# Optimization experiments

Measured on AMD Instinct MI355X. Metric: run time of the kernel, lower is better.

## Reference

```python
import jax, jax.numpy as jnp
import numpy as np

N, F, O, E = 2048, 128, 128, 16


def setup_inputs() -> dict:
    key = jax.random.key(0)
    ks = jax.random.split(key, 6)
    x = jax.random.normal(ks[0], (N, F), dtype=jnp.float32)
    # two supports (normalized adjacency-like dense matrices)
    support = jax.random.uniform(ks[1], (2, N, N), dtype=jnp.float32)
    edge_feature = jax.random.normal(ks[2], (N, N, E), dtype=jnp.float32)
    # glorot-ish scale for edge weight and dense weights
    weight_edge = jax.random.normal(ks[3], (N, N, E), dtype=jnp.float32) * 0.05
    bias_edge = jnp.zeros((N, N), dtype=jnp.float32)
    glorot = float(np.sqrt(6.0 / (F + O)))
    w0 = jax.random.uniform(ks[4], (F, O), dtype=jnp.float32, minval=-glorot, maxval=glorot)
    w1 = jax.random.uniform(ks[5], (F, O), dtype=jnp.float32, minval=-glorot, maxval=glorot)
    b = jnp.zeros((O,), dtype=jnp.float32)
    return {"x": x, "support": support, "edge_feature": edge_feature,
            "weight_edge": weight_edge, "bias_edge": bias_edge,
            "w0": w0, "w1": w1, "b": b}


def reference(x, support, edge_feature, weight_edge, bias_edge, w0, w1, b):
    # support branch 0: plain GCN propagation  (SpMM expressed dense)
    pre0 = x @ w0                      # [N, O]
    s0 = support[0] @ pre0             # [N, O]
    # support branch 1: edge-feature gated propagation
    pre1 = x @ w1                      # [N, O]
    # per-pair dot of edge features with per-pair weights -> [N, N] gate
    edge = jax.nn.sigmoid(jnp.einsum('nme,nme->nm', edge_feature, weight_edge) + bias_edge)
    s1 = (edge * support[1]) @ pre1    # gated adjacency matmul, [N, O]
    out = s0 + s1 + b                  # add_n + bias
    return jax.nn.relu(out)
```

## Files before the change

kernel.cpp:

```cpp
#include <hip/hip_runtime.h>
#include <math.h>

#define N 2048
#define F 128
#define O 128
#define E 16

#define BK 32
#define GBN 16
#define GKC 8
#define GMK (N / GKC)
#define GSTEPS (GMK / BK)

typedef __attribute__((ext_vector_type(8))) short          shortx8;
typedef __attribute__((ext_vector_type(8))) unsigned short u16x8;
typedef __attribute__((ext_vector_type(4))) float          floatx4;

static __device__ __forceinline__ unsigned short f2bf(float f) {
    unsigned int u = __float_as_uint(f);
    unsigned int r = (u + 0x7FFFu + ((u >> 16) & 1u)) >> 16;
    return (unsigned short)r;
}

__global__ __launch_bounds__(128)
void pre_gemm(const float* __restrict__ x,
              const float* __restrict__ w0,
              const float* __restrict__ w1,
              unsigned short* __restrict__ pre_bf) {
    const int n = blockIdx.x;
    const int b = blockIdx.y;
    const int o = threadIdx.x;
    const float* __restrict__ w = b ? w1 : w0;
    __shared__ float xs[F];
    xs[o] = x[(size_t)n * F + o];
    __syncthreads();
    float acc = 0.f;
#pragma unroll 8
    for (int k = 0; k < F; ++k)
        acc += xs[k] * w[(size_t)k * O + o];
    pre_bf[(size_t)b * N * O + (size_t)n * O + o] = f2bf(acc);
}

__global__ __launch_bounds__(256)
void transpose_pre(const unsigned short* __restrict__ pre_bf,
                   unsigned short* __restrict__ preT) {
    __shared__ unsigned short tile[64][65];
    const int n0 = blockIdx.x * 64, o0 = blockIdx.y * 64;
    const size_t base = (size_t)blockIdx.z * N * O;
    const int t = threadIdx.x;
    const int r = t >> 2, q = t & 3;
    const unsigned short* src = pre_bf + base + (size_t)(n0 + r) * O + o0 + q * 16;
    u16x8 v0 = *(const u16x8*)(src);
    u16x8 v1 = *(const u16x8*)(src + 8);
#pragma unroll
    for (int j = 0; j < 8; ++j) {
        tile[q * 16 + j][r]     = v0[j];
        tile[q * 16 + 8 + j][r] = v1[j];
    }
    __syncthreads();
    u16x8 w0v, w1v;
#pragma unroll
    for (int j = 0; j < 8; ++j) {
        w0v[j] = tile[r][q * 16 + j];
        w1v[j] = tile[r][q * 16 + 8 + j];
    }
    unsigned short* dst = preT + base + (size_t)(o0 + r) * N + n0 + q * 16;
    *(u16x8*)(dst)     = w0v;
    *(u16x8*)(dst + 8) = w1v;
}

__global__ __launch_bounds__(256)
void gate_kernel(const float* __restrict__ ef,
                 const float* __restrict__ we,
                 const float* __restrict__ be,
                 const float* __restrict__ sup1,
                 unsigned short* __restrict__ G) {
    const size_t tid  = (size_t)blockIdx.x * 256 + threadIdx.x;
    const size_t pair = tid >> 2;
    const int    sub  = (int)(threadIdx.x & 3);
    const float4 e4 = ((const float4*)ef)[pair * 4 + sub];
    const float4 w4 = ((const float4*)we)[pair * 4 + sub];
    float v = e4.x * w4.x + e4.y * w4.y + e4.z * w4.z + e4.w * w4.w;
    v += __shfl_xor(v, 1);
    v += __shfl_xor(v, 2);
    if (sub == 0) {
        const float t = v + be[pair];
        const float g = (1.f / (1.f + __expf(-t))) * sup1[pair];
        G[pair] = f2bf(g);
    }
}

__global__ __launch_bounds__(256)
void dual_gemm(const float* __restrict__ S0,
               const unsigned short* __restrict__ G,
               const unsigned short* __restrict__ preT,
               float* __restrict__ partial) {
    const int t    = threadIdx.x;
    const int lane = t & 63;
    const int w    = t >> 6;
    const int rb   = blockIdx.x & 127;
    const int kc   = blockIdx.x >> 7;
    const int n0   = rb * GBN;
    const int m_b  = kc * GMK;

    const int row  = lane & 15;
    const int kg   = lane >> 4;
    const int col0 = w * 32 + row;

    const float*          aS = S0   + (size_t)(n0 + row) * N + m_b + kg * 8;
    const unsigned short* aG = G    + (size_t)(n0 + row) * N + m_b + kg * 8;
    const unsigned short* b0 = preT + (size_t)col0 * N            + m_b + kg * 8;
    const unsigned short* b1 = b0   + (size_t)16 * N;
    const unsigned short* c0 = b0   + (size_t)O * N;
    const unsigned short* c1 = b1   + (size_t)O * N;

    floatx4 acc0 = {0.f, 0.f, 0.f, 0.f};
    floatx4 acc1 = {0.f, 0.f, 0.f, 0.f};

#pragma unroll 2
    for (int s = 0; s < GSTEPS; ++s) {
        const int mo = s * BK;
        const float4 f0 = *(const float4*)(aS + mo);
        const float4 f1 = *(const float4*)(aS + mo + 4);
        const shortx8 a_g = *(const shortx8*)(aG + mo);
        const shortx8 b00 = *(const shortx8*)(b0 + mo);
        const shortx8 b01 = *(const shortx8*)(b1 + mo);
        const shortx8 b10 = *(const shortx8*)(c0 + mo);
        const shortx8 b11 = *(const shortx8*)(c1 + mo);
        shortx8 a_s;
        a_s[0] = (short)f2bf(f0.x); a_s[1] = (short)f2bf(f0.y);
        a_s[2] = (short)f2bf(f0.z); a_s[3] = (short)f2bf(f0.w);
        a_s[4] = (short)f2bf(f1.x); a_s[5] = (short)f2bf(f1.y);
        a_s[6] = (short)f2bf(f1.z); a_s[7] = (short)f2bf(f1.w);
        acc0 = __builtin_amdgcn_mfma_f32_16x16x32_bf16(a_s, b00, acc0, 0, 0, 0);
        acc0 = __builtin_amdgcn_mfma_f32_16x16x32_bf16(a_g, b10, acc0, 0, 0, 0);
        acc1 = __builtin_amdgcn_mfma_f32_16x16x32_bf16(a_s, b01, acc1, 0, 0, 0);
        acc1 = __builtin_amdgcn_mfma_f32_16x16x32_bf16(a_g, b11, acc1, 0, 0, 0);
    }

    float* dst = partial + (size_t)kc * (N * O)
               + (size_t)(n0 + kg * 4) * O + w * 32 + row;
#pragma unroll
    for (int j = 0; j < 4; ++j) {
        dst[(size_t)j * O]      = acc0[j];
        dst[(size_t)j * O + 16] = acc1[j];
    }
}

__global__ __launch_bounds__(256)
void reduce_out(const float* __restrict__ partial,
                const float* __restrict__ bias,
                float* __restrict__ out) {
    const int i4 = blockIdx.x * 256 + threadIdx.x;
    const float4* p = (const float4*)partial;
    float4 r = p[i4];
#pragma unroll
    for (int j = 1; j < GKC; ++j) {
        const float4 a = p[i4 + (size_t)j * (N * O / 4)];
        r.x += a.x; r.y += a.y; r.z += a.z; r.w += a.w;
    }
    const float4 bb = ((const float4*)bias)[i4 & (O / 4 - 1)];
    float4 o;
    o.x = fmaxf(r.x + bb.x, 0.f);
    o.y = fmaxf(r.y + bb.y, 0.f);
    o.z = fmaxf(r.z + bb.z, 0.f);
    o.w = fmaxf(r.w + bb.w, 0.f);
    ((float4*)out)[i4] = o;
}

extern "C" void kernel_launch(void* const* d_in, const int* in_sizes, int n_in,
                              void* d_out, int out_size, void* d_ws, size_t ws_size,
                              hipStream_t stream) {
    const float* x   = (const float*)d_in[0];
    const float* sup = (const float*)d_in[1];
    const float* ef  = (const float*)d_in[2];
    const float* we  = (const float*)d_in[3];
    const float* be  = (const float*)d_in[4];
    const float* w0  = (const float*)d_in[5];
    const float* w1  = (const float*)d_in[6];
    const float* b   = (const float*)d_in[7];
    float* out = (float*)d_out;

    unsigned short* preT   = (unsigned short*)d_ws;
    unsigned short* G      = preT + 2 * (size_t)N * O;
    float*          partial = (float*)(G + (size_t)N * N);
    unsigned short* pre_bf = (unsigned short*)partial;

    pre_gemm<<<dim3(N, 2), 128, 0, stream>>>(x, w0, w1, pre_bf);
    transpose_pre<<<dim3(N / 64, O / 64, 2), 256, 0, stream>>>(pre_bf, preT);
    gate_kernel<<<(unsigned)((size_t)N * N * 4 / 256), 256, 0, stream>>>(
        ef, we, be, sup + (size_t)N * N, G);
    dual_gemm<<<GKC * 128, 256, 0, stream>>>(sup, G, preT, partial);
    reduce_out<<<N * O / 4 / 256, 256, 0, stream>>>(partial, b, out);
}
```

Before: 143.3 us.

## Fuse pre-GEMM with transpose via MFMA and do split-K reduction in-block

Replaces the scalar pre_gemm plus separate transpose kernel with one MFMA kernel that stages a bf16 transposed weight tile in LDS and writes the transposed pre-activation directly. The dual GEMM now splits K across the four waves of a block and reduces through shared memory, applying bias and ReLU in the same kernel. This removes the partial-sum buffer round trip and the reduce kernel, so two launches go away. Each block now covers only 32 output columns, so the S0 and G rows are re-read by four column-group blocks; a block index swizzle is added to improve cache locality for those re-reads.

```diff
diff --git a/kernel.cpp b/kernel.cpp
--- a/kernel.cpp
+++ b/kernel.cpp
@@ -6,14 +6,9 @@
 #define O 128
 #define E 16
 
-#define BK 32
-#define GBN 16
-#define GKC 8
-#define GMK (N / GKC)
-#define GSTEPS (GMK / BK)
-
 typedef __attribute__((ext_vector_type(8))) short          shortx8;
 typedef __attribute__((ext_vector_type(8))) unsigned short u16x8;
+typedef __attribute__((ext_vector_type(4))) unsigned short u16x4;
 typedef __attribute__((ext_vector_type(4))) float          floatx4;
 
 static __device__ __forceinline__ unsigned short f2bf(float f) {
@@ -22,51 +17,56 @@
     return (unsigned short)r;
 }
 
-__global__ __launch_bounds__(128)
-void pre_gemm(const float* __restrict__ x,
-              const float* __restrict__ w0,
-              const float* __restrict__ w1,
-              unsigned short* __restrict__ pre_bf) {
-    const int n = blockIdx.x;
-    const int b = blockIdx.y;
-    const int o = threadIdx.x;
-    const float* __restrict__ w = b ? w1 : w0;
-    __shared__ float xs[F];
-    xs[o] = x[(size_t)n * F + o];
-    __syncthreads();
-    float acc = 0.f;
-#pragma unroll 8
-    for (int k = 0; k < F; ++k)
-        acc += xs[k] * w[(size_t)k * O + o];
-    pre_bf[(size_t)b * N * O + (size_t)n * O + o] = f2bf(acc);
-}
+__global__ __launch_bounds__(256)
+void pre_t(const float* __restrict__ x,
+           const float* __restrict__ w0,
+           const float* __restrict__ w1,
+           unsigned short* __restrict__ preT) {
+    __shared__ unsigned short wT[128 * 136];
+    const int t  = threadIdx.x;
+    const int n0 = blockIdx.x * 16;
+    const int b  = blockIdx.y;
+    const float* __restrict__ wsrc = b ? w1 : w0;
 
-__global__ __launch_bounds__(256)
-void transpose_pre(const unsigned short* __restrict__ pre_bf,
-                   unsigned short* __restrict__ preT) {
-    __shared__ unsigned short tile[64][65];
-    const int n0 = blockIdx.x * 64, o0 = blockIdx.y * 64;
-    const size_t base = (size_t)blockIdx.z * N * O;
-    const int t = threadIdx.x;
-    const int r = t >> 2, q = t & 3;
-    const unsigned short* src = pre_bf + base + (size_t)(n0 + r) * O + o0 + q * 16;
-    u16x8 v0 = *(const u16x8*)(src);
-    u16x8 v1 = *(const u16x8*)(src + 8);
 #pragma unroll
-    for (int j = 0; j < 8; ++j) {
-        tile[q * 16 + j][r]     = v0[j];
-        tile[q * 16 + 8 + j][r] = v1[j];
+    for (int i = 0; i < 64; ++i) {
+        const int idx = i * 256 + t;
+        const int k = idx >> 7, o = idx & 127;
+        wT[o * 136 + k] = f2bf(wsrc[idx]);
     }
     __syncthreads();
-    u16x8 w0v, w1v;
+
+    const int lane = t & 63;
+    const int wv   = t >> 6;
+    const int row  = lane & 15;
+    const int kg   = lane >> 4;
+    const int col0 = wv * 32 + row;
+
+    floatx4 acc0 = {0.f, 0.f, 0.f, 0.f};
+    floatx4 acc1 = {0.f, 0.f, 0.f, 0.f};
+
 #pragma unroll
-    for (int j = 0; j < 8; ++j) {
-        w0v[j] = tile[r][q * 16 + j];
-        w1v[j] = tile[r][q * 16 + 8 + j];
+    for (int kk = 0; kk < 4; ++kk) {
+        const float* xp = x + (size_t)(n0 + row) * F + kk * 32 + kg * 8;
+        const float4 f0 = *(const float4*)(xp);
+        const float4 f1 = *(const float4*)(xp + 4);
+        shortx8 a;
+        a[0] = (short)f2bf(f0.x); a[1] = (short)f2bf(f0.y);
+        a[2] = (short)f2bf(f0.z); a[3] = (short)f2bf(f0.w);
+        a[4] = (short)f2bf(f1.x); a[5] = (short)f2bf(f1.y);
+        a[6] = (short)f2bf(f1.z); a[7] = (short)f2bf(f1.w);
+        const shortx8 bA = *(const shortx8*)(wT + col0 * 136 + kk * 32 + kg * 8);
+        const shortx8 bB = *(const shortx8*)(wT + (col0 + 16) * 136 + kk * 32 + kg * 8);
+        acc0 = __builtin_amdgcn_mfma_f32_16x16x32_bf16(a, bA, acc0, 0, 0, 0);
+        acc1 = __builtin_amdgcn_mfma_f32_16x16x32_bf16(a, bB, acc1, 0, 0, 0);
     }
-    unsigned short* dst = preT + base + (size_t)(o0 + r) * N + n0 + q * 16;
-    *(u16x8*)(dst)     = w0v;
-    *(u16x8*)(dst + 8) = w1v;
+
+    const int prow = kg * 4;
+    u16x4 s0, s1;
+#pragma unroll
+    for (int j = 0; j < 4; ++j) { s0[j] = f2bf(acc0[j]); s1[j] = f2bf(acc1[j]); }
+    *(u16x4*)(preT + ((size_t)b * O + col0) * N + n0 + prow)      = s0;
+    *(u16x4*)(preT + ((size_t)b * O + col0 + 16) * N + n0 + prow) = s1;
 }
 
 __global__ __launch_bounds__(256)
@@ -91,35 +91,40 @@
 }
 
 __global__ __launch_bounds__(256)
-void dual_gemm(const float* __restrict__ S0,
-               const unsigned short* __restrict__ G,
-               const unsigned short* __restrict__ preT,
-               float* __restrict__ partial) {
+void gemm_direct(const float* __restrict__ S0,
+                 const unsigned short* __restrict__ G,
+                 const unsigned short* __restrict__ preT,
+                 const float* __restrict__ bias,
+                 float* __restrict__ out) {
+    __shared__ float red[4][16][36];
+
+    const int bx   = blockIdx.x;
+    const int orig = (bx & 7) * 64 + (bx >> 3);
+    const int rb   = orig >> 2;
+    const int cg   = orig & 3;
+    const int n0   = rb * 16;
+
     const int t    = threadIdx.x;
     const int lane = t & 63;
-    const int w    = t >> 6;
-    const int rb   = blockIdx.x & 127;
-    const int kc   = blockIdx.x >> 7;
-    const int n0   = rb * GBN;
-    const int m_b  = kc * GMK;
-
+    const int wv   = t >> 6;
+    const int m_b  = wv * 512;
     const int row  = lane & 15;
     const int kg   = lane >> 4;
-    const int col0 = w * 32 + row;
+    const int col0 = cg * 32 + row;
 
     const float*          aS = S0   + (size_t)(n0 + row) * N + m_b + kg * 8;
     const unsigned short* aG = G    + (size_t)(n0 + row) * N + m_b + kg * 8;
-    const unsigned short* b0 = preT + (size_t)col0 * N            + m_b + kg * 8;
-    const unsigned short* b1 = b0   + (size_t)16 * N;
-    const unsigned short* c0 = b0   + (size_t)O * N;
-    const unsigned short* c1 = b1   + (size_t)O * N;
+    const unsigned short* b0 = preT + (size_t)col0 * N        + m_b + kg * 8;
+    const unsigned short* b1 = b0 + (size_t)16 * N;
+    const unsigned short* c0 = b0 + (size_t)O * N;
+    const unsigned short* c1 = b1 + (size_t)O * N;
 
     floatx4 acc0 = {0.f, 0.f, 0.f, 0.f};
     floatx4 acc1 = {0.f, 0.f, 0.f, 0.f};
 
 #pragma unroll 2
-    for (int s = 0; s < GSTEPS; ++s) {
-        const int mo = s * BK;
+    for (int s = 0; s < 16; ++s) {
+        const int mo = s * 32;
         const float4 f0 = *(const float4*)(aS + mo);
         const float4 f1 = *(const float4*)(aS + mo + 4);
         const shortx8 a_g = *(const shortx8*)(aG + mo);
@@ -138,34 +143,22 @@
         acc1 = __builtin_amdgcn_mfma_f32_16x16x32_bf16(a_g, b11, acc1, 0, 0, 0);
     }
 
-    float* dst = partial + (size_t)kc * (N * O)
-               + (size_t)(n0 + kg * 4) * O + w * 32 + row;
+    const int prow = kg * 4;
 #pragma unroll
     for (int j = 0; j < 4; ++j) {
-        dst[(size_t)j * O]      = acc0[j];
-        dst[(size_t)j * O + 16] = acc1[j];
+        red[wv][prow + j][row]      = acc0[j];
+        red[wv][prow + j][16 + row] = acc1[j];
     }
-}
+    __syncthreads();
 
-__global__ __launch_bounds__(256)
-void reduce_out(const float* __restrict__ partial,
-                const float* __restrict__ bias,
-                float* __restrict__ out) {
-    const int i4 = blockIdx.x * 256 + threadIdx.x;
-    const float4* p = (const float4*)partial;
-    float4 r = p[i4];
-#pragma unroll
-    for (int j = 1; j < GKC; ++j) {
-        const float4 a = p[i4 + (size_t)j * (N * O / 4)];
-        r.x += a.x; r.y += a.y; r.z += a.z; r.w += a.w;
-    }
-    const float4 bb = ((const float4*)bias)[i4 & (O / 4 - 1)];
-    float4 o;
-    o.x = fmaxf(r.x + bb.x, 0.f);
-    o.y = fmaxf(r.y + bb.y, 0.f);
-    o.z = fmaxf(r.z + bb.z, 0.f);
-    o.w = fmaxf(r.w + bb.w, 0.f);
-    ((float4*)out)[i4] = o;
+    const int r = t >> 4;
+    const int c = (t & 15) * 2;
+    float v0 = red[0][r][c]     + red[1][r][c]     + red[2][r][c]     + red[3][r][c];
+    float v1 = red[0][r][c + 1] + red[1][r][c + 1] + red[2][r][c + 1] + red[3][r][c + 1];
+    v0 = fmaxf(v0 + bias[cg * 32 + c],     0.f);
+    v1 = fmaxf(v1 + bias[cg * 32 + c + 1], 0.f);
+    float2 o2; o2.x = v0; o2.y = v1;
+    *(float2*)(out + (size_t)(n0 + r) * O + cg * 32 + c) = o2;
 }
 
 extern "C" void kernel_launch(void* const* d_in, const int* in_sizes, int n_in,
@@ -181,15 +174,11 @@
     const float* b   = (const float*)d_in[7];
     float* out = (float*)d_out;
 
-    unsigned short* preT   = (unsigned short*)d_ws;
-    unsigned short* G      = preT + 2 * (size_t)N * O;
-    float*          partial = (float*)(G + (size_t)N * N);
-    unsigned short* pre_bf = (unsigned short*)partial;
+    unsigned short* preT = (unsigned short*)d_ws;
+    unsigned short* G    = preT + 2 * (size_t)N * O;
 
-    pre_gemm<<<dim3(N, 2), 128, 0, stream>>>(x, w0, w1, pre_bf);
-    transpose_pre<<<dim3(N / 64, O / 64, 2), 256, 0, stream>>>(pre_bf, preT);
+    pre_t<<<dim3(N / 16, 2), 256, 0, stream>>>(x, w0, w1, preT);
     gate_kernel<<<(unsigned)((size_t)N * N * 4 / 256), 256, 0, stream>>>(
         ef, we, be, sup + (size_t)N * N, G);
-    dual_gemm<<<GKC * 128, 256, 0, stream>>>(sup, G, preT, partial);
-    reduce_out<<<N * O / 4 / 256, 256, 0, stream>>>(partial, b, out);
+    gemm_direct<<<512, 256, 0, stream>>>(sup, G, preT, b, out);
 }
```

Result: faster. 138.1 us (-3.6%).
